# Performance work log

Hardware: AMD Instinct MI355X
Metric: run time of the kernel (lower is better)

The kernel has to match this reference:

```python
import jax, jax.numpy as jnp
import numpy as np

C = 512  # n_channels

def _maxpool2x2(t):
    # t: [B, C, H, W] -> [B, C, H//2, W//2]
    B, Cc, H, W = t.shape
    return t.reshape(B, Cc, H // 2, 2, W // 2, 2).max(axis=(3, 5))

def setup_inputs() -> dict:
    key = jax.random.key(0)
    ks = jax.random.split(key, 6)
    B, H, W = 16, 64, 64
    x = jax.random.normal(ks[0], (B, C, H, W), dtype=jnp.float32)
    # 1x1 conv weights (spectral-normalized convs, no bias) stored as [out, in]
    wq = jax.random.normal(ks[1], (C // 8, C), dtype=jnp.float32) * 0.05
    wk = jax.random.normal(ks[2], (C // 8, C), dtype=jnp.float32) * 0.05
    wv = jax.random.normal(ks[3], (C // 2, C), dtype=jnp.float32) * 0.05
    wo = jax.random.normal(ks[4], (C, C // 2), dtype=jnp.float32) * 0.05
    gamma = jnp.zeros((1,), dtype=jnp.float32) + 0.5  # nonzero so output depends on attention path
    return {"x": x, "wq": wq, "wk": wk, "wv": wv, "wo": wo, "gamma": gamma}

def reference(x, wq, wk, wv, wo, gamma):
    B, Cc, H, W = x.shape
    n = H * W
    # 1x1 convs are channel-mixing matmuls
    f = jnp.einsum('oc,bchw->bohw', wq, x).reshape(B, Cc // 8, n)            # [B, C/8, n]
    g = _maxpool2x2(jnp.einsum('oc,bchw->bohw', wk, x)).reshape(B, Cc // 8, n // 4)  # [B, C/8, n/4]
    h = _maxpool2x2(jnp.einsum('oc,bchw->bohw', wv, x)).reshape(B, Cc // 2, n // 4)  # [B, C/2, n/4]
    # attention: softmax over pooled kv positions
    beta = jax.nn.softmax(jnp.einsum('bcn,bcm->bnm', f, g), axis=-1)         # [B, n, n/4]
    o = jnp.einsum('bcm,bnm->bcn', h, beta).reshape(B, Cc // 2, H, W)        # [B, C/2, H, W]
    o = jnp.einsum('oc,bchw->bohw', wo, o)                                   # [B, C, H, W]
    return gamma.reshape(()) * o + x
```

## Files before the change

kernel.cpp:

```cpp
#include <hip/hip_runtime.h>
#include <cstdint>
#include <cstddef>

namespace {

constexpr int kB  = 16;
constexpr int kC  = 512;
constexpr int kCQ = 64;
constexpr int kCV = 256;
constexpr int kN  = 4096;
constexpr int kM  = 1024;

typedef _Float16 f16;
typedef _Float16 f16x8 __attribute__((ext_vector_type(8)));
typedef float    f32x4 __attribute__((ext_vector_type(4)));

__device__ __forceinline__ void gload16(const f16* g, f16* l) {
    __builtin_amdgcn_global_load_lds(
        (const __attribute__((address_space(1))) void*)g,
        (__attribute__((address_space(3))) void*)l,
        16, 0, 0);
}

__global__ __launch_bounds__(256)
void convert_weights_kernel(const float* __restrict__ wq,
                            const float* __restrict__ wk,
                            const float* __restrict__ wv,
                            const float* __restrict__ wo,
                            const float* __restrict__ gamma,
                            f16* __restrict__ wcat,
                            f16* __restrict__ woh)
{
    const int idx = blockIdx.x * 256 + threadIdx.x;
    if (idx < 49152) {
        const int e = idx * 4;
        const int r = e >> 9, c = e & 511;
        const float* src = (r < 64)  ? (wq + ((size_t)r << 9))
                         : (r < 128) ? (wk + ((size_t)(r - 64) << 9))
                                     : (wv + ((size_t)(r - 128) << 9));
        float4 v = *(const float4*)(src + c);
        union { f16 h4[4]; uint2 u; } pk;
        pk.h4[0] = (f16)v.x; pk.h4[1] = (f16)v.y;
        pk.h4[2] = (f16)v.z; pk.h4[3] = (f16)v.w;
        *(uint2*)(wcat + e) = pk.u;
    } else {
        const int e = (idx - 49152) * 4;
        const float g = gamma[0];
        float4 v = *(const float4*)(wo + e);
        union { f16 h4[4]; uint2 u; } pk;
        pk.h4[0] = (f16)(g * v.x); pk.h4[1] = (f16)(g * v.y);
        pk.h4[2] = (f16)(g * v.z); pk.h4[3] = (f16)(g * v.w);
        *(uint2*)(woh + e) = pk.u;
    }
}

__global__ __launch_bounds__(512, 4)
void proj_pool_mfma(const float* __restrict__ x,
                    const f16* __restrict__ wcat,
                    f16* __restrict__ fT,
                    f16* __restrict__ gT,
                    f16* __restrict__ h)
{
    const int nt  = blockIdx.x;
    const int mt  = blockIdx.y;
    const int b   = blockIdx.z;
    const int tid = threadIdx.x;
    const int w    = tid >> 6;
    const int lane = tid & 63;
    const int quad = lane >> 4;
    const int lq   = lane & 15;
    const int wr   = w >> 1;
    const int wc   = w & 1;

    __shared__ alignas(16) f16 As[2][192 * 32];
    __shared__ alignas(16) f16 Bs[2][128 * 36];

    const f16*   Ab = wcat + (size_t)mt * 192 * kC;
    const float* Xb = x + (size_t)b * kC * kN + nt * 128;

    f32x4 acc[3][4];
#pragma unroll
    for (int i = 0; i < 3; ++i)
#pragma unroll
        for (int j = 0; j < 4; ++j) acc[i][j] = {0.f, 0.f, 0.f, 0.f};

    const int bn = tid & 127;
    const int kg = tid >> 7;
    float xv[8];

    auto stageA = [&](int buf, int k0) {
        {
            const int u = tid;
            const int row = u >> 2, g = u & 3;
            gload16(Ab + (size_t)row * kC + k0 + ((g ^ (row & 3)) * 8),
                    &As[buf][(w * 64) * 8]);
        }
        if (tid < 256) {
            const int u = 512 + tid;
            const int row = u >> 2, g = u & 3;
            gload16(Ab + (size_t)row * kC + k0 + ((g ^ (row & 3)) * 8),
                    &As[buf][(512 + w * 64) * 8]);
        }
    };
    auto loadB = [&](int k0) {
#pragma unroll
        for (int j = 0; j < 8; ++j) xv[j] = Xb[(size_t)(k0 + kg * 8 + j) * kN + bn];
    };
    auto writeB = [&](int buf) {
        union { f16 hh[8]; uint4 u; } pk;
#pragma unroll
        for (int j = 0; j < 8; ++j) pk.hh[j] = (f16)xv[j];
        *(uint4*)&Bs[buf][bn * 36 + kg * 8] = pk.u;
    };

    stageA(0, 0);
    loadB(0);
    writeB(0);
    __syncthreads();

    for (int ks = 0; ks < 16; ++ks) {
        const int cur = ks & 1;
        if (ks < 15) {
            stageA(cur ^ 1, (ks + 1) * 32);
            loadB((ks + 1) * 32);
        }

        f16x8 bsv[4];
#pragma unroll
        for (int tj = 0; tj < 4; ++tj) {
            const int col = (tj < 2) ? (wc * 32 + tj * 16 + lq)
                                     : (64 + wc * 32 + (tj - 2) * 16 + lq);
            bsv[tj] = *(const f16x8*)&Bs[cur][col * 36 + quad * 8];
        }
        __builtin_amdgcn_s_setprio(1);
#pragma unroll
        for (int ti = 0; ti < 3; ++ti) {
            const int row = wr * 48 + ti * 16 + lq;
            const f16x8 af = *(const f16x8*)&As[cur][row * 32 + ((quad ^ (row & 3)) * 8)];
#pragma unroll
            for (int tj = 0; tj < 4; ++tj)
                acc[ti][tj] = __builtin_amdgcn_mfma_f32_16x16x32_f16(
                    af, bsv[tj], acc[ti][tj], 0, 0, 0);
        }
        __builtin_amdgcn_s_setprio(0);

        if (ks < 15) writeB(cur ^ 1);
        __syncthreads();
    }

#pragma unroll
    for (int ti = 0; ti < 3; ++ti) {
        const int ch0 = mt * 192 + wr * 48 + ti * 16;
        if (ch0 < 64) {
            f16* fb = fT + (size_t)b * kN * kCQ;
#pragma unroll
            for (int tj = 0; tj < 4; ++tj) {
                const int col = (tj < 2) ? (wc * 32 + tj * 16 + lq)
                                         : (64 + wc * 32 + (tj - 2) * 16 + lq);
                const int n = nt * 128 + col;
                union { f16 h4[4]; uint2 u; } pk;
#pragma unroll
                for (int r = 0; r < 4; ++r) pk.h4[r] = (f16)acc[ti][tj][r];
                *(uint2*)(fb + (size_t)n * kCQ + ch0 + quad * 4) = pk.u;
            }
        } else {
#pragma unroll
            for (int tjp = 0; tjp < 2; ++tjp) {
                float p[4];
#pragma unroll
                for (int r = 0; r < 4; ++r) {
                    float v = fmaxf(acc[ti][tjp][r], acc[ti][tjp + 2][r]);
                    v = fmaxf(v, __shfl_xor(v, 1, 64));
                    p[r] = v;
                }
                const int m = nt * 32 + wc * 16 + tjp * 8 + (lq >> 1);
                if ((lq & 1) == 0) {
                    if (ch0 < 128) {
                        union { f16 h4[4]; uint2 u; } pk;
#pragma unroll
                        for (int r = 0; r < 4; ++r) pk.h4[r] = (f16)p[r];
                        *(uint2*)(gT + ((size_t)b * kM + m) * kCQ + (ch0 - 64) + quad * 4) = pk.u;
                    } else {
#pragma unroll
                        for (int r = 0; r < 4; ++r) {
                            const int ch = ch0 - 128 + quad * 4 + r;
                            h[((size_t)b * kCV + ch) * kM + m] = (f16)p[r];
                        }
                    }
                }
            }
        }
    }
}

__global__ __launch_bounds__(256, 3)
void attn_out_kernel(const f16* __restrict__ fT,
                     const f16* __restrict__ gT,
                     const f16* __restrict__ hmat,
                     const f16* __restrict__ woh,
                     const float* __restrict__ x,
                     float* __restrict__ out)
{
    const int qt   = blockIdx.x;
    const int b    = blockIdx.y;
    const int tid  = threadIdx.x;
    const int w    = tid >> 6;
    const int lane = tid & 63;
    const int quad = lane >> 4;
    const int lq   = lane & 15;

    __shared__ union alignas(16) SMem {
        struct {
            f16 gs[2][32 * 64];
            f16 hs[2][256 * 32];
            f16 ps[64 * 36];
        } p1;
        struct {
            f16 osT[64 * 260];
        } p2;
    } sm;

    const int q = qt * 64 + w * 16 + lq;
    const f16* fq = fT + ((size_t)b * kN + q) * kCQ;
    const f16x8 af0 = *(const f16x8*)(fq + quad * 8);
    const f16x8 af1 = *(const f16x8*)(fq + 32 + quad * 8);

    float m_run = -3.0e38f, l_run = 0.f;
    f32x4 o_acc[16];
#pragma unroll
    for (int ci = 0; ci < 16; ++ci) o_acc[ci] = {0.f, 0.f, 0.f, 0.f};

    const f16* gTb = gT + (size_t)b * kM * kCQ;
    const f16* hb  = hmat + (size_t)b * kCV * kM;

    auto stage = [&](int buf, int m0) {
        {
            const int m = tid >> 3, g = tid & 7;
            gload16(gTb + (size_t)(m0 + m) * kCQ + ((g ^ (m & 7)) * 8),
                    &sm.p1.gs[buf][(w * 64) * 8]);
        }
#pragma unroll
        for (int p = 0; p < 4; ++p) {
            const int u = p * 256 + tid;
            const int c = u >> 2, g = u & 3;
            gload16(hb + (size_t)c * kM + m0 + ((g ^ (c & 3)) * 8),
                    &sm.p1.hs[buf][(p * 256 + w * 64) * 8]);
        }
    };

    stage(0, 0);
    __syncthreads();

    for (int mi = 0; mi < 32; ++mi) {
        const int cur = mi & 1;
        if (mi < 31) stage(cur ^ 1, (mi + 1) * 32);

        const int mr0 = lq, mr1 = 16 + lq;
        const f16* gsc = &sm.p1.gs[cur][0];
        const f16x8 bg00 = *(const f16x8*)&gsc[mr0 * 64 + ((quad       ^ (mr0 & 7)) * 8)];
        const f16x8 bg01 = *(const f16x8*)&gsc[mr0 * 64 + (((4 + quad) ^ (mr0 & 7)) * 8)];
        const f16x8 bg10 = *(const f16x8*)&gsc[mr1 * 64 + ((quad       ^ (mr1 & 7)) * 8)];
        const f16x8 bg11 = *(const f16x8*)&gsc[mr1 * 64 + (((4 + quad) ^ (mr1 & 7)) * 8)];
        f32x4 s0 = {0.f, 0.f, 0.f, 0.f}, s1 = {0.f, 0.f, 0.f, 0.f};
        s0 = __builtin_amdgcn_mfma_f32_16x16x32_f16(bg00, af0, s0, 0, 0, 0);
        s0 = __builtin_amdgcn_mfma_f32_16x16x32_f16(bg01, af1, s0, 0, 0, 0);
        s1 = __builtin_amdgcn_mfma_f32_16x16x32_f16(bg10, af0, s1, 0, 0, 0);
        s1 = __builtin_amdgcn_mfma_f32_16x16x32_f16(bg11, af1, s1, 0, 0, 0);

        float cm = fmaxf(fmaxf(fmaxf(s0[0], s0[1]), fmaxf(s0[2], s0[3])),
                         fmaxf(fmaxf(s1[0], s1[1]), fmaxf(s1[2], s1[3])));
        cm = fmaxf(cm, __shfl_xor(cm, 16, 64));
        cm = fmaxf(cm, __shfl_xor(cm, 32, 64));
        const float nm = fmaxf(m_run, cm);
        const float al = __expf(m_run - nm);
        float e0[4], e1[4];
#pragma unroll
        for (int r = 0; r < 4; ++r) { e0[r] = __expf(s0[r] - nm); e1[r] = __expf(s1[r] - nm); }
        float psum = (e0[0] + e0[1]) + (e0[2] + e0[3]) + (e1[0] + e1[1]) + (e1[2] + e1[3]);
        psum += __shfl_xor(psum, 16, 64);
        psum += __shfl_xor(psum, 32, 64);
        m_run = nm;
        l_run = l_run * al + psum;

        union { f16 h4[4]; uint2 u; } pk0, pk1;
#pragma unroll
        for (int r = 0; r < 4; ++r) { pk0.h4[r] = (f16)e0[r]; pk1.h4[r] = (f16)e1[r]; }
        *(uint2*)&sm.p1.ps[(w * 16 + lq) * 36 + quad * 4]      = pk0.u;
        *(uint2*)&sm.p1.ps[(w * 16 + lq) * 36 + 16 + quad * 4] = pk1.u;
        __builtin_amdgcn_sched_barrier(0);
        const f16x8 bp = *(const f16x8*)&sm.p1.ps[(w * 16 + lq) * 36 + quad * 8];

        __builtin_amdgcn_s_setprio(1);
#pragma unroll
        for (int ci = 0; ci < 16; ++ci) {
            const int c = ci * 16 + lq;
            const f16x8 ha = *(const f16x8*)&sm.p1.hs[cur][c * 32 + ((quad ^ (lq & 3)) * 8)];
            o_acc[ci] *= al;
            o_acc[ci] = __builtin_amdgcn_mfma_f32_16x16x32_f16(ha, bp, o_acc[ci], 0, 0, 0);
        }
        __builtin_amdgcn_s_setprio(0);

        __syncthreads();
    }

    const float inv = 1.0f / l_run;
#pragma unroll
    for (int ci = 0; ci < 16; ++ci) {
        union { f16 h4[4]; uint2 u; } pk;
#pragma unroll
        for (int r = 0; r < 4; ++r) pk.h4[r] = (f16)(o_acc[ci][r] * inv);
        *(uint2*)&sm.p2.osT[(w * 16 + lq) * 260 + ci * 16 + quad * 4] = pk.u;
    }

    for (int half = 0; half < 2; ++half) {
        f32x4 acc2[16];
#pragma unroll
        for (int os = 0; os < 16; ++os) acc2[os] = {0.f, 0.f, 0.f, 0.f};

        for (int ck = 0; ck < 8; ++ck) {
            const f16x8 bo = *(const f16x8*)&sm.p2.osT[(w * 16 + lq) * 260 + ck * 32 + quad * 8];
            __builtin_amdgcn_s_setprio(1);
#pragma unroll
            for (int os = 0; os < 16; ++os) {
                const f16x8 wa = *(const f16x8*)(woh +
                    (size_t)(half * 256 + os * 16 + lq) * 256 + ck * 32 + quad * 8);
                acc2[os] = __builtin_amdgcn_mfma_f32_16x16x32_f16(wa, bo, acc2[os], 0, 0, 0);
            }
            __builtin_amdgcn_s_setprio(0);
        }

        const int n0 = qt * 64 + w * 16 + lq;
#pragma unroll
        for (int os = 0; os < 16; ++os) {
#pragma unroll
            for (int r = 0; r < 4; ++r) {
                const int oc = half * 256 + os * 16 + quad * 4 + r;
                const size_t idx = ((size_t)b * kC + oc) * (size_t)kN + n0;
                out[idx] = acc2[os][r] + x[idx];
            }
        }
    }
}

}

extern "C" void kernel_launch(void* const* d_in, const int* in_sizes, int n_in,
                              void* d_out, int out_size, void* d_ws, size_t ws_size,
                              hipStream_t stream) {
    const float* x     = (const float*)d_in[0];
    const float* wq    = (const float*)d_in[1];
    const float* wk    = (const float*)d_in[2];
    const float* wv    = (const float*)d_in[3];
    const float* wo    = (const float*)d_in[4];
    const float* gamma = (const float*)d_in[5];
    float* out = (float*)d_out;

    f16* fT   = (f16*)d_ws;
    f16* gT   = fT  + (size_t)kB * kN * kCQ;
    f16* hw   = gT  + (size_t)kB * kM * kCQ;
    f16* woh  = hw  + (size_t)kB * kCV * kM;
    f16* wcat = woh + (size_t)kC * kCV;

    hipLaunchKernelGGL(convert_weights_kernel, dim3(320), dim3(256), 0, stream,
                       wq, wk, wv, wo, gamma, wcat, woh);
    hipLaunchKernelGGL(proj_pool_mfma, dim3(32, 2, kB), dim3(512), 0, stream,
                       x, wcat, fT, gT, hw);
    hipLaunchKernelGGL(attn_out_kernel, dim3(64, kB), dim3(256), 0, stream,
                       fT, gT, hw, woh, x, out);
}
```

Before: 532.9 us.

## Replace direct-to-LDS async loads with register-staged prefetch and direct weight reads

In the projection kernel, the A (weight) tile is no longer staged through LDS with global_load_lds; each wave reads its weight fragments straight from global memory, relying on cache. In the attention kernel, the double-buffered direct-to-LDS staging of g and h is replaced by register prefetch into a single LDS buffer, with a padded h layout instead of the XOR swizzle, and two barriers per iteration. This trades async LDS DMA and double buffering for simpler register staging and lower LDS use, but adds barriers and puts global-load latency on the MFMA path in the projection kernel.

```diff
diff --git a/kernel.cpp b/kernel.cpp
--- a/kernel.cpp
+++ b/kernel.cpp
@@ -14,13 +14,6 @@
 typedef _Float16 f16;
 typedef _Float16 f16x8 __attribute__((ext_vector_type(8)));
 typedef float    f32x4 __attribute__((ext_vector_type(4)));
-
-__device__ __forceinline__ void gload16(const f16* g, f16* l) {
-    __builtin_amdgcn_global_load_lds(
-        (const __attribute__((address_space(1))) void*)g,
-        (__attribute__((address_space(3))) void*)l,
-        16, 0, 0);
-}
 
 __global__ __launch_bounds__(256)
 void convert_weights_kernel(const float* __restrict__ wq,
@@ -72,7 +65,6 @@
     const int wr   = w >> 1;
     const int wc   = w & 1;
 
-    __shared__ alignas(16) f16 As[2][192 * 32];
     __shared__ alignas(16) f16 Bs[2][128 * 36];
 
     const f16*   Ab = wcat + (size_t)mt * 192 * kC;
@@ -88,20 +80,6 @@
     const int kg = tid >> 7;
     float xv[8];
 
-    auto stageA = [&](int buf, int k0) {
-        {
-            const int u = tid;
-            const int row = u >> 2, g = u & 3;
-            gload16(Ab + (size_t)row * kC + k0 + ((g ^ (row & 3)) * 8),
-                    &As[buf][(w * 64) * 8]);
-        }
-        if (tid < 256) {
-            const int u = 512 + tid;
-            const int row = u >> 2, g = u & 3;
-            gload16(Ab + (size_t)row * kC + k0 + ((g ^ (row & 3)) * 8),
-                    &As[buf][(512 + w * 64) * 8]);
-        }
-    };
     auto loadB = [&](int k0) {
 #pragma unroll
         for (int j = 0; j < 8; ++j) xv[j] = Xb[(size_t)(k0 + kg * 8 + j) * kN + bn];
@@ -113,17 +91,13 @@
         *(uint4*)&Bs[buf][bn * 36 + kg * 8] = pk.u;
     };
 
-    stageA(0, 0);
     loadB(0);
     writeB(0);
     __syncthreads();
 
     for (int ks = 0; ks < 16; ++ks) {
         const int cur = ks & 1;
-        if (ks < 15) {
-            stageA(cur ^ 1, (ks + 1) * 32);
-            loadB((ks + 1) * 32);
-        }
+        if (ks < 15) loadB((ks + 1) * 32);
 
         f16x8 bsv[4];
 #pragma unroll
@@ -136,7 +110,7 @@
 #pragma unroll
         for (int ti = 0; ti < 3; ++ti) {
             const int row = wr * 48 + ti * 16 + lq;
-            const f16x8 af = *(const f16x8*)&As[cur][row * 32 + ((quad ^ (row & 3)) * 8)];
+            const f16x8 af = *(const f16x8*)(Ab + (size_t)row * kC + ks * 32 + quad * 8);
 #pragma unroll
             for (int tj = 0; tj < 4; ++tj)
                 acc[ti][tj] = __builtin_amdgcn_mfma_f32_16x16x32_f16(
@@ -211,8 +185,8 @@
 
     __shared__ union alignas(16) SMem {
         struct {
-            f16 gs[2][32 * 64];
-            f16 hs[2][256 * 32];
+            f16 gsT[32 * 64];
+            f16 hs[256 * 40];
             f16 ps[64 * 36];
         } p1;
         struct {
@@ -233,34 +207,34 @@
     const f16* gTb = gT + (size_t)b * kM * kCQ;
     const f16* hb  = hmat + (size_t)b * kCV * kM;
 
-    auto stage = [&](int buf, int m0) {
-        {
-            const int m = tid >> 3, g = tid & 7;
-            gload16(gTb + (size_t)(m0 + m) * kCQ + ((g ^ (m & 7)) * 8),
-                    &sm.p1.gs[buf][(w * 64) * 8]);
-        }
-#pragma unroll
-        for (int p = 0; p < 4; ++p) {
-            const int u = p * 256 + tid;
-            const int c = u >> 2, g = u & 3;
-            gload16(hb + (size_t)c * kM + m0 + ((g ^ (c & 3)) * 8),
-                    &sm.p1.hs[buf][(p * 256 + w * 64) * 8]);
-        }
-    };
-
-    stage(0, 0);
-    __syncthreads();
+    const int gm = tid >> 3, gsu = tid & 7, ggu = gsu ^ (gm & 7);
+    const int hc = tid >> 2, hu = tid & 3;
+    uint4 pg, ph[4];
+    pg = *(const uint4*)(gTb + (size_t)gm * kCQ + ggu * 8);
+#pragma unroll
+    for (int p = 0; p < 4; ++p)
+        ph[p] = *(const uint4*)(hb + (size_t)(hc + p * 64) * kM + hu * 8);
 
     for (int mi = 0; mi < 32; ++mi) {
-        const int cur = mi & 1;
-        if (mi < 31) stage(cur ^ 1, (mi + 1) * 32);
+        __syncthreads();
+        *(uint4*)&sm.p1.gsT[gm * 64 + gsu * 8] = pg;
+#pragma unroll
+        for (int p = 0; p < 4; ++p)
+            *(uint4*)&sm.p1.hs[(hc + p * 64) * 40 + hu * 8] = ph[p];
+        __syncthreads();
+        if (mi < 31) {
+            const int m1 = (mi + 1) * 32;
+            pg = *(const uint4*)(gTb + (size_t)(m1 + gm) * kCQ + ggu * 8);
+#pragma unroll
+            for (int p = 0; p < 4; ++p)
+                ph[p] = *(const uint4*)(hb + (size_t)(hc + p * 64) * kM + m1 + hu * 8);
+        }
 
         const int mr0 = lq, mr1 = 16 + lq;
-        const f16* gsc = &sm.p1.gs[cur][0];
-        const f16x8 bg00 = *(const f16x8*)&gsc[mr0 * 64 + ((quad       ^ (mr0 & 7)) * 8)];
-        const f16x8 bg01 = *(const f16x8*)&gsc[mr0 * 64 + (((4 + quad) ^ (mr0 & 7)) * 8)];
-        const f16x8 bg10 = *(const f16x8*)&gsc[mr1 * 64 + ((quad       ^ (mr1 & 7)) * 8)];
-        const f16x8 bg11 = *(const f16x8*)&gsc[mr1 * 64 + (((4 + quad) ^ (mr1 & 7)) * 8)];
+        const f16x8 bg00 = *(const f16x8*)&sm.p1.gsT[mr0 * 64 + ((quad       ^ (mr0 & 7)) * 8)];
+        const f16x8 bg01 = *(const f16x8*)&sm.p1.gsT[mr0 * 64 + (((4 + quad) ^ (mr0 & 7)) * 8)];
+        const f16x8 bg10 = *(const f16x8*)&sm.p1.gsT[mr1 * 64 + ((quad       ^ (mr1 & 7)) * 8)];
+        const f16x8 bg11 = *(const f16x8*)&sm.p1.gsT[mr1 * 64 + (((4 + quad) ^ (mr1 & 7)) * 8)];
         f32x4 s0 = {0.f, 0.f, 0.f, 0.f}, s1 = {0.f, 0.f, 0.f, 0.f};
         s0 = __builtin_amdgcn_mfma_f32_16x16x32_f16(bg00, af0, s0, 0, 0, 0);
         s0 = __builtin_amdgcn_mfma_f32_16x16x32_f16(bg01, af1, s0, 0, 0, 0);
@@ -293,17 +267,16 @@
         __builtin_amdgcn_s_setprio(1);
 #pragma unroll
         for (int ci = 0; ci < 16; ++ci) {
-            const int c = ci * 16 + lq;
-            const f16x8 ha = *(const f16x8*)&sm.p1.hs[cur][c * 32 + ((quad ^ (lq & 3)) * 8)];
+            const f16x8 ha = *(const f16x8*)&sm.p1.hs[(ci * 16 + lq) * 40 + quad * 8];
             o_acc[ci] *= al;
             o_acc[ci] = __builtin_amdgcn_mfma_f32_16x16x32_f16(ha, bp, o_acc[ci], 0, 0, 0);
         }
         __builtin_amdgcn_s_setprio(0);
-
-        __syncthreads();
     }
 
     const float inv = 1.0f / l_run;
+    __syncthreads();
+
 #pragma unroll
     for (int ci = 0; ci < 16; ++ci) {
         union { f16 h4[4]; uint2 u; } pk;
```

Measured after the change: 731.8 us. 37.3% more time.
